# Performance work log

Hardware: AMD Instinct MI355X
Metric: run time of the kernel (lower is better)

The kernel has to match this reference:

```python
import jax, jax.numpy as jnp
import numpy as np

N_EXPERTS = 256
N_GROUP = 8
TOPK_GROUP = 4
TOP_K = 8
NORM_TOPK_PROB = True
ROUTED_SCALING_FACTOR = 2.5
NUM_TOKENS = 262144


def setup_inputs() -> dict:
    key = jax.random.key(0)
    k1, k2 = jax.random.split(key)
    router_logits = jax.random.normal(k1, (NUM_TOKENS, N_EXPERTS), dtype=jnp.float32)
    e_score_correction_bias = jax.random.normal(k2, (N_EXPERTS,), dtype=jnp.float32) * 0.1
    return {"router_logits": router_logits, "e_score_correction_bias": e_score_correction_bias}


def reference(router_logits, e_score_correction_bias):
    experts_per_group = N_EXPERTS // N_GROUP  # 32
    scores = jax.nn.sigmoid(router_logits)                       # [T, E]
    scores_for_choice = scores + e_score_correction_bias          # [T, E]

    # group score = sum of top-2 expert scores within each group
    grouped = scores_for_choice.reshape(-1, N_GROUP, experts_per_group)  # [T, G, E/G]
    top2_vals, _ = jax.lax.top_k(grouped, 2)                      # [T, G, 2]
    group_scores = top2_vals.sum(axis=-1)                         # [T, G]

    # keep top `TOPK_GROUP` groups
    _, group_idx = jax.lax.top_k(group_scores, TOPK_GROUP)        # [T, topk_group]
    group_mask = jnp.sum(jax.nn.one_hot(group_idx, N_GROUP, dtype=jnp.bool_), axis=1)  # [T, G]
    score_mask = jnp.repeat(group_mask, experts_per_group, axis=-1)  # [T, E]

    masked_scores = jnp.where(score_mask, scores_for_choice, 0.0)
    _, topk_indices = jax.lax.top_k(masked_scores, TOP_K)         # [T, top_k]

    topk_weights = jnp.take_along_axis(scores, topk_indices, axis=-1)  # [T, top_k]
    if NORM_TOPK_PROB:
        denom = topk_weights.sum(axis=-1, keepdims=True) + 1e-20
        topk_weights = topk_weights / denom
    topk_weights = topk_weights * ROUTED_SCALING_FACTOR
    return topk_indices, topk_weights
```

## Files before the change

kernel.cpp:

```cpp
#include <hip/hip_runtime.h>
#include <stdint.h>

#define NE 256
#define TKG 4
#define TK 8
#define TPB 64
#define CDW 76
#define CNT_OFF 72

typedef float pf2 __attribute__((ext_vector_type(2)));

__device__ __forceinline__ pf2 pk_fma_ss(pf2 a, pf2 b, pf2 cs) {
    pf2 d; asm("v_pk_fma_f32 %0, %1, %2, %3" : "=v"(d) : "v"(a), "v"(b), "s"(cs)); return d;
}
__device__ __forceinline__ pf2 pk_fma_sv(pf2 as, pf2 b, pf2 c) {
    pf2 d; asm("v_pk_fma_f32 %0, %1, %2, %3" : "=v"(d) : "s"(as), "v"(b), "v"(c)); return d;
}
__device__ __forceinline__ pf2 pk_fma_vv(pf2 a, pf2 b, pf2 c) {
    pf2 d; asm("v_pk_fma_f32 %0, %1, %2, %3" : "=v"(d) : "v"(a), "v"(b), "v"(c)); return d;
}
__device__ __forceinline__ pf2 pk_mul_s(pf2 a, pf2 bs) {
    pf2 d; asm("v_pk_mul_f32 %0, %1, %2" : "=v"(d) : "v"(a), "s"(bs)); return d;
}
__device__ __forceinline__ pf2 pk_mul_v(pf2 a, pf2 b) {
    pf2 d; asm("v_pk_mul_f32 %0, %1, %2" : "=v"(d) : "v"(a), "v"(b)); return d;
}
__device__ __forceinline__ pf2 pk_add_s(pf2 a, pf2 bs) {
    pf2 d; asm("v_pk_add_f32 %0, %1, %2" : "=v"(d) : "v"(a), "s"(bs)); return d;
}

__device__ __forceinline__ pf2 np_expf2(pf2 v) {
    const pf2 LOG2E  = {1.44269504088896341f, 1.44269504088896341f};
    const pf2 NLN2HI = {-0.693359375f, -0.693359375f};
    const pf2 LN2LO  = {2.12194440e-4f, 2.12194440e-4f};
    const pf2 A0     = {1.9875691500E-4f, 1.9875691500E-4f};
    const pf2 A1     = {1.3981999507E-3f, 1.3981999507E-3f};
    const pf2 A2     = {8.3334519073E-3f, 8.3334519073E-3f};
    const pf2 A3     = {4.1665795894E-2f, 4.1665795894E-2f};
    const pf2 A4     = {1.6666665459E-1f, 1.6666665459E-1f};
    const pf2 A5     = {5.0000001201E-1f, 5.0000001201E-1f};
    const pf2 ONE    = {1.0f, 1.0f};

    pf2 m = pk_mul_s(v, LOG2E);
    pf2 q; q.x = rintf(m.x); q.y = rintf(m.y);
    pf2 t = pk_fma_sv(NLN2HI, q, v);
    t = pk_fma_sv(LN2LO, q, t);
    pf2 t2 = pk_mul_v(t, t);
    pf2 p = pk_fma_sv(A0, t, A1);
    p = pk_fma_ss(p, t, A2);
    p = pk_fma_ss(p, t, A3);
    p = pk_fma_ss(p, t, A4);
    p = pk_fma_ss(p, t, A5);
    p = pk_fma_vv(p, t2, t);
    p = pk_add_s(p, ONE);
    pf2 r;
    r.x = ldexpf(p.x, (int)q.x);
    r.y = ldexpf(p.y, (int)q.y);
    return r;
}

__device__ __forceinline__ float crdiv1(float d) {
    float y0 = __builtin_amdgcn_rcpf(d);
    float e0 = fmaf(-d, y0, 1.0f);
    float y1 = fmaf(e0, y0, y0);
    float e1 = fmaf(-d, y1, 1.0f);
    float y2 = fmaf(e1, y1, y1);
    float r  = fmaf(-d, y2, 1.0f);
    return fmaf(r, y2, y2);
}

__device__ __forceinline__ unsigned ordkey(float v) {
    int b = __float_as_int(v);
    return (unsigned)(b ^ ((b >> 31) | 0x80000000));
}
__device__ __forceinline__ float inv_ordkey(unsigned u) {
    unsigned b = (u & 0x80000000u) ? (u ^ 0x80000000u) : ~u;
    return __uint_as_float(b);
}

__device__ __forceinline__ float rlanef(float v, int l) {
    return __int_as_float(__builtin_amdgcn_readlane(__float_as_int(v), l));
}
__device__ __forceinline__ unsigned rlaneu(unsigned v, int l) {
    return (unsigned)__builtin_amdgcn_readlane((int)v, l);
}
__device__ __forceinline__ unsigned umax_(unsigned a, unsigned b) { return a > b ? a : b; }
__device__ __forceinline__ int mbcnt64(unsigned long long m) {
    return __builtin_amdgcn_mbcnt_hi((unsigned)(m >> 32),
           __builtin_amdgcn_mbcnt_lo((unsigned)m, 0u));
}

template <int CTRL>
__device__ __forceinline__ float dppf(float x) {
    int xi = __float_as_int(x);
    return __int_as_float(__builtin_amdgcn_update_dpp(xi, xi, CTRL, 0xF, 0xF, false));
}
#define DPP_XOR1  0xB1
#define DPP_XOR2  0x4E
#define DPP_HMIRR 0x141
#define DPP_ROR8  0x128
#define DPP_BC15  0x142
#define DPP_BC31  0x143

#define INS8(cand) do {                                                \
    const uint64_t c_ = (cand);                                        \
    const bool q0 = c_ > v0, q1 = c_ > v1, q2 = c_ > v2, q3 = c_ > v3; \
    const bool q4 = c_ > v4, q5 = c_ > v5, q6 = c_ > v6, q7 = c_ > v7; \
    v7 = q7 ? (q6 ? v6 : c_) : v7;                                     \
    v6 = q6 ? (q5 ? v5 : c_) : v6;                                     \
    v5 = q5 ? (q4 ? v4 : c_) : v5;                                     \
    v4 = q4 ? (q3 ? v3 : c_) : v4;                                     \
    v3 = q3 ? (q2 ? v2 : c_) : v3;                                     \
    v2 = q2 ? (q1 ? v1 : c_) : v2;                                     \
    v1 = q1 ? (q0 ? v0 : c_) : v1;                                     \
    v0 = q0 ? c_ : v0;                                                 \
} while (0)

__device__ __forceinline__ void score_token(
    const float4 cur, const pf2 biasL, const pf2 biasH,
    const int lane, const int bpa, uint32_t* row)
{
    const pf2 ONE = {1.0f, 1.0f};
    pf2 eA = np_expf2((pf2){-cur.x, -cur.y});
    pf2 eB = np_expf2((pf2){-cur.z, -cur.w});
    pf2 dA = pk_add_s(eA, ONE);
    pf2 dB = pk_add_s(eB, ONE);
    const float s0 = crdiv1(dA.x);
    const float s1 = crdiv1(dA.y);
    const float s2 = crdiv1(dB.x);
    const float s3 = crdiv1(dB.y);
    const float c0 = s0 + biasL.x;
    const float c1 = s1 + biasL.y;
    const float c2 = s2 + biasH.x;
    const float c3 = s3 + biasH.y;

    float a1 = fmaxf(c0, c1), a2 = fminf(c0, c1);
    float d1 = fmaxf(c2, c3), d2 = fminf(c2, c3);
    float m1 = fmaxf(a1, d1);
    float m2 = fmaxf(fminf(a1, d1), fmaxf(a2, d2));

    {
        float p1 = dppf<DPP_XOR1>(m1), p2 = dppf<DPP_XOR1>(m2);
        float n1 = fmaxf(m1, p1);
        m2 = fmaxf(fminf(m1, p1), fmaxf(m2, p2)); m1 = n1;
    }
    {
        float p1 = dppf<DPP_XOR2>(m1), p2 = dppf<DPP_XOR2>(m2);
        float n1 = fmaxf(m1, p1);
        m2 = fmaxf(fminf(m1, p1), fmaxf(m2, p2)); m1 = n1;
    }
    {
        float p1 = dppf<DPP_HMIRR>(m1), p2 = dppf<DPP_HMIRR>(m2);
        float n1 = fmaxf(m1, p1);
        m2 = fmaxf(fminf(m1, p1), fmaxf(m2, p2)); m1 = n1;
    }
    const float gs = m1 + m2;

    const float gb = __int_as_float(
        __builtin_amdgcn_ds_bpermute(bpa, __float_as_int(gs)));
    const unsigned long long gtm = __ballot(gb > gs);
    const unsigned long long eqm = __ballot(gb == gs);
    const unsigned long long term = gtm | (eqm & 0x7F3F1F0F07030100ull);
    unsigned km8 = 0;
    #pragma unroll
    for (int a = 0; a < 8; ++a)
        km8 |= (unsigned)(__popcll((term >> (8 * a)) & 0xFFull) < 4 ? 1u : 0u) << a;
    const int g = lane >> 3;
    const bool keep = (km8 >> g) & 1u;

    const float inf_ = __uint_as_float(0x7F800000u);
    float mm = keep ? m2 : inf_;
    mm = fminf(mm, dppf<DPP_ROR8>(mm));
    mm = fminf(mm, dppf<DPP_BC15>(mm));
    mm = fminf(mm, dppf<DPP_BC31>(mm));
    const float t0f = rlanef(mm, 63);

    const bool cd0 = keep && (c0 >= t0f);
    const bool cd1 = keep && (c1 >= t0f);
    const bool cd2 = keep && (c2 >= t0f);
    const bool cd3 = keep && (c3 >= t0f);
    const unsigned long long b0 = __ballot(cd0);
    const unsigned long long b1 = __ballot(cd1);
    const unsigned long long b2 = __ballot(cd2);
    const unsigned long long b3 = __ballot(cd3);
    const unsigned p1_ = __popcll(b0);
    const unsigned p2_ = p1_ + __popcll(b1);
    const unsigned p3_ = p2_ + __popcll(b2);
    unsigned cnt = p3_ + __popcll(b3);

    const unsigned k0 = ordkey(c0);
    const unsigned k1 = ordkey(c1);
    const unsigned k2 = ordkey(c2);
    const unsigned k3 = ordkey(c3);

    const int base = lane * 4;
    if (cnt <= 32u) {
        if (cd0) *reinterpret_cast<uint64_t*>(&row[2 * (0u  + mbcnt64(b0))]) =
            ((uint64_t)k0 << 32) | (unsigned)(255 - base);
        if (cd1) *reinterpret_cast<uint64_t*>(&row[2 * (p1_ + mbcnt64(b1))]) =
            ((uint64_t)k1 << 32) | (unsigned)(255 - base - 1);
        if (cd2) *reinterpret_cast<uint64_t*>(&row[2 * (p2_ + mbcnt64(b2))]) =
            ((uint64_t)k2 << 32) | (unsigned)(255 - base - 2);
        if (cd3) *reinterpret_cast<uint64_t*>(&row[2 * (p3_ + mbcnt64(b3))]) =
            ((uint64_t)k3 << 32) | (unsigned)(255 - base - 3);
    } else {
        unsigned mk0 = keep ? k0 : 0x80000000u;
        unsigned mk1 = keep ? k1 : 0x80000000u;
        unsigned mk2 = keep ? k2 : 0x80000000u;
        unsigned mk3 = keep ? k3 : 0x80000000u;
        for (int r = 0; r < TK; ++r) {
            unsigned h = umax_(umax_(mk0, mk1), umax_(mk2, mk3));
            unsigned m = h;
            m = umax_(m, (unsigned)__shfl_xor((int)m, 1));
            m = umax_(m, (unsigned)__shfl_xor((int)m, 2));
            m = umax_(m, (unsigned)__shfl_xor((int)m, 4));
            m = umax_(m, (unsigned)__shfl_xor((int)m, 8));
            const unsigned M = umax_(umax_(rlaneu(m, 0), rlaneu(m, 16)),
                                     umax_(rlaneu(m, 32), rlaneu(m, 48)));
            const unsigned long long bl = __ballot(h == M);
            const int wl = __ffsll(bl) - 1;
            const unsigned long long sb0 = __ballot(mk0 == M);
            const unsigned long long sb1 = __ballot(mk1 == M);
            const unsigned long long sb2 = __ballot(mk2 == M);
            const int slot = ((sb0 >> wl) & 1) ? 0 : ((sb1 >> wl) & 1) ? 1
                           : ((sb2 >> wl) & 1) ? 2 : 3;
            if (lane == r)
                *reinterpret_cast<uint64_t*>(&row[2 * r]) =
                    ((uint64_t)M << 32) | (unsigned)(255 - (wl * 4 + slot));
            const bool iw = (lane == wl);
            mk0 = (iw && slot == 0) ? 0u : mk0;
            mk1 = (iw && slot == 1) ? 0u : mk1;
            mk2 = (iw && slot == 2) ? 0u : mk2;
            mk3 = (iw && slot == 3) ? 0u : mk3;
        }
        cnt = 8;
    }
    if (lane < 4)
        *reinterpret_cast<uint64_t*>(&row[2 * (cnt + lane)]) = 0ull;
    if (lane == 0) row[CNT_OFF] = cnt;
}

__global__ __launch_bounds__(256, 4) void route_kernel(
    const float* __restrict__ logits,
    const float* __restrict__ bias,
    float* __restrict__ out_idx_f,
    float* __restrict__ out_w,
    int T)
{
    __shared__ uint32_t cand[TPB * CDW];
    __shared__ float    bias_s[NE];

    const int lane = threadIdx.x & 63;
    const int wvi  = threadIdx.x >> 6;
    const long long tok0 = (long long)blockIdx.x * TPB;

    bias_s[threadIdx.x] = bias[threadIdx.x];

    {
        const float4 bias4 = *reinterpret_cast<const float4*>(bias + lane * 4);
        const pf2 biasL = {bias4.x, bias4.y};
        const pf2 biasH = {bias4.z, bias4.w};
        const float* lp = logits + (tok0 + wvi * 16) * NE + lane * 4;
        uint32_t* wrow = &cand[(wvi * 16) * CDW];
        const int bpa = (lane & 7) << 5;

        float4 cA = *reinterpret_cast<const float4*>(lp);
        float4 cB = *reinterpret_cast<const float4*>(lp + NE);
        float4 nA, nB;
        for (int i = 0; i < 8; ++i) {
            if (i < 7) {
                nA = *reinterpret_cast<const float4*>(lp + (2 * i + 2) * NE);
                nB = *reinterpret_cast<const float4*>(lp + (2 * i + 3) * NE);
            }
            score_token(cA, biasL, biasH, lane, bpa, wrow + (2 * i) * CDW);
            score_token(cB, biasL, biasH, lane, bpa, wrow + (2 * i + 1) * CDW);
            cA = nA; cB = nB;
        }
    }
    __syncthreads();

    if (threadIdx.x < TPB) {
        uint32_t* row = &cand[threadIdx.x * CDW];
        const long long t = tok0 + threadIdx.x;
        const unsigned cnt = row[CNT_OFF];
        const unsigned iters = (cnt + 3) >> 2;

        uint64_t v0 = 0, v1 = 0, v2 = 0, v3 = 0, v4 = 0, v5 = 0, v6 = 0, v7 = 0;
        const ulonglong2* rp = reinterpret_cast<const ulonglong2*>(row);
        for (unsigned it = 0; it < iters; ++it) {
            const ulonglong2 a = rp[2 * it];
            const ulonglong2 b = rp[2 * it + 1];
            INS8(a.x); INS8(a.y); INS8(b.x); INS8(b.y);
        }

        const int e0 = 255 - (int)(v0 & 255u);
        const int e1 = 255 - (int)(v1 & 255u);
        const int e2 = 255 - (int)(v2 & 255u);
        const int e3 = 255 - (int)(v3 & 255u);
        const int e4 = 255 - (int)(v4 & 255u);
        const int e5 = 255 - (int)(v5 & 255u);
        const int e6 = 255 - (int)(v6 & 255u);
        const int e7 = 255 - (int)(v7 & 255u);
        const float s0 = inv_ordkey((unsigned)(v0 >> 32)) - bias_s[e0];
        const float s1 = inv_ordkey((unsigned)(v1 >> 32)) - bias_s[e1];
        const float s2 = inv_ordkey((unsigned)(v2 >> 32)) - bias_s[e2];
        const float s3 = inv_ordkey((unsigned)(v3 >> 32)) - bias_s[e3];
        const float s4 = inv_ordkey((unsigned)(v4 >> 32)) - bias_s[e4];
        const float s5 = inv_ordkey((unsigned)(v5 >> 32)) - bias_s[e5];
        const float s6 = inv_ordkey((unsigned)(v6 >> 32)) - bias_s[e6];
        const float s7 = inv_ordkey((unsigned)(v7 >> 32)) - bias_s[e7];

        const float denom = ((s0 + s1) + (s2 + s3)) + ((s4 + s5) + (s6 + s7));
        const float scale = 2.5f * __builtin_amdgcn_rcpf(denom + 1e-20f);

        float4* oi = reinterpret_cast<float4*>(out_idx_f + t * TK);
        float4* ow = reinterpret_cast<float4*>(out_w + t * TK);
        oi[0] = make_float4((float)e0, (float)e1, (float)e2, (float)e3);
        oi[1] = make_float4((float)e4, (float)e5, (float)e6, (float)e7);
        ow[0] = make_float4(s0 * scale, s1 * scale, s2 * scale, s3 * scale);
        ow[1] = make_float4(s4 * scale, s5 * scale, s6 * scale, s7 * scale);
    }
}

extern "C" void kernel_launch(void* const* d_in, const int* in_sizes, int n_in,
                              void* d_out, int out_size, void* d_ws, size_t ws_size,
                              hipStream_t stream) {
    const float* logits = (const float*)d_in[0];
    const float* bias   = (const float*)d_in[1];
    const int T = in_sizes[0] / NE;

    float* out_idx_f = (float*)d_out;
    float* out_w     = (float*)d_out + (size_t)T * TK;

    const int grid = T / TPB;
    route_kernel<<<grid, 256, 0, stream>>>(logits, bias, out_idx_f, out_w, T);
}
```

Baseline: 90.59 us.

## Process two tokens per wavefront with 8 experts per lane

Reworks the per-token scoring so each 64-lane wavefront handles two tokens at once, with each half-wave of 32 lanes owning one token and each lane holding 8 consecutive experts instead of 4. Group top-2 reduction now needs only two DPP steps, and group ranking uses two bpermutes with half-wave ballots. This halves the number of cross-lane reduction and ballot sequences per token. In exchange it raises per-lane register use, makes the prefix and rank bookkeeping more complex, and adds a serialized slow fallback path for each half.

```diff
diff --git a/kernel.cpp b/kernel.cpp
--- a/kernel.cpp
+++ b/kernel.cpp
@@ -2,7 +2,6 @@
 #include <stdint.h>
 
 #define NE 256
-#define TKG 4
 #define TK 8
 #define TPB 64
 #define CDW 76
@@ -84,6 +83,9 @@
 __device__ __forceinline__ unsigned rlaneu(unsigned v, int l) {
     return (unsigned)__builtin_amdgcn_readlane((int)v, l);
 }
+__device__ __forceinline__ unsigned rlaneu_s(unsigned v, int l) {
+    return (unsigned)__builtin_amdgcn_readlane((int)v, l);
+}
 __device__ __forceinline__ unsigned umax_(unsigned a, unsigned b) { return a > b ? a : b; }
 __device__ __forceinline__ int mbcnt64(unsigned long long m) {
     return __builtin_amdgcn_mbcnt_hi((unsigned)(m >> 32),
@@ -97,10 +99,8 @@
 }
 #define DPP_XOR1  0xB1
 #define DPP_XOR2  0x4E
-#define DPP_HMIRR 0x141
+#define DPP_ROR4  0x124
 #define DPP_ROR8  0x128
-#define DPP_BC15  0x142
-#define DPP_BC31  0x143
 
 #define INS8(cand) do {                                                \
     const uint64_t c_ = (cand);                                        \
@@ -116,128 +116,197 @@
     v0 = q0 ? c_ : v0;                                                 \
 } while (0)
 
-__device__ __forceinline__ void score_token(
-    const float4 cur, const pf2 biasL, const pf2 biasH,
-    const int lane, const int bpa, uint32_t* row)
+__device__ __forceinline__ void score_pair(
+    const float4 xa, const float4 xb,
+    const pf2 bp0, const pf2 bp1, const pf2 bp2, const pf2 bp3,
+    const int lane, const int bpa1,
+    uint32_t* rowA, uint32_t* rowB, uint32_t* rowMine)
 {
+    const int l31 = lane & 31;
+    const int h   = lane >> 5;
+
     const pf2 ONE = {1.0f, 1.0f};
-    pf2 eA = np_expf2((pf2){-cur.x, -cur.y});
-    pf2 eB = np_expf2((pf2){-cur.z, -cur.w});
+    pf2 eA = np_expf2((pf2){-xa.x, -xa.y});
+    pf2 eB = np_expf2((pf2){-xa.z, -xa.w});
+    pf2 eC = np_expf2((pf2){-xb.x, -xb.y});
+    pf2 eD = np_expf2((pf2){-xb.z, -xb.w});
     pf2 dA = pk_add_s(eA, ONE);
     pf2 dB = pk_add_s(eB, ONE);
-    const float s0 = crdiv1(dA.x);
-    const float s1 = crdiv1(dA.y);
-    const float s2 = crdiv1(dB.x);
-    const float s3 = crdiv1(dB.y);
-    const float c0 = s0 + biasL.x;
-    const float c1 = s1 + biasL.y;
-    const float c2 = s2 + biasH.x;
-    const float c3 = s3 + biasH.y;
+    pf2 dC = pk_add_s(eC, ONE);
+    pf2 dD = pk_add_s(eD, ONE);
+    const float s0 = crdiv1(dA.x), s1 = crdiv1(dA.y);
+    const float s2 = crdiv1(dB.x), s3 = crdiv1(dB.y);
+    const float s4 = crdiv1(dC.x), s5 = crdiv1(dC.y);
+    const float s6 = crdiv1(dD.x), s7 = crdiv1(dD.y);
+    const float c0 = s0 + bp0.x, c1 = s1 + bp0.y;
+    const float c2 = s2 + bp1.x, c3 = s3 + bp1.y;
+    const float c4 = s4 + bp2.x, c5 = s5 + bp2.y;
+    const float c6 = s6 + bp3.x, c7 = s7 + bp3.y;
 
     float a1 = fmaxf(c0, c1), a2 = fminf(c0, c1);
-    float d1 = fmaxf(c2, c3), d2 = fminf(c2, c3);
-    float m1 = fmaxf(a1, d1);
-    float m2 = fmaxf(fminf(a1, d1), fmaxf(a2, d2));
+    float b1 = fmaxf(c2, c3), b2 = fminf(c2, c3);
+    float t1 = fmaxf(a1, b1), t2 = fmaxf(fminf(a1, b1), fmaxf(a2, b2));
+    float p1 = fmaxf(c4, c5), p2 = fminf(c4, c5);
+    float q1 = fmaxf(c6, c7), q2 = fminf(c6, c7);
+    float u1 = fmaxf(p1, q1), u2 = fmaxf(fminf(p1, q1), fmaxf(p2, q2));
+    float m1 = fmaxf(t1, u1), m2 = fmaxf(fminf(t1, u1), fmaxf(t2, u2));
 
     {
-        float p1 = dppf<DPP_XOR1>(m1), p2 = dppf<DPP_XOR1>(m2);
-        float n1 = fmaxf(m1, p1);
-        m2 = fmaxf(fminf(m1, p1), fmaxf(m2, p2)); m1 = n1;
+        float px1 = dppf<DPP_XOR1>(m1), px2 = dppf<DPP_XOR1>(m2);
+        float n1 = fmaxf(m1, px1);
+        m2 = fmaxf(fminf(m1, px1), fmaxf(m2, px2)); m1 = n1;
     }
     {
-        float p1 = dppf<DPP_XOR2>(m1), p2 = dppf<DPP_XOR2>(m2);
-        float n1 = fmaxf(m1, p1);
-        m2 = fmaxf(fminf(m1, p1), fmaxf(m2, p2)); m1 = n1;
-    }
-    {
-        float p1 = dppf<DPP_HMIRR>(m1), p2 = dppf<DPP_HMIRR>(m2);
-        float n1 = fmaxf(m1, p1);
-        m2 = fmaxf(fminf(m1, p1), fmaxf(m2, p2)); m1 = n1;
+        float px1 = dppf<DPP_XOR2>(m1), px2 = dppf<DPP_XOR2>(m2);
+        float n1 = fmaxf(m1, px1);
+        m2 = fmaxf(fminf(m1, px1), fmaxf(m2, px2)); m1 = n1;
     }
     const float gs = m1 + m2;
 
-    const float gb = __int_as_float(
-        __builtin_amdgcn_ds_bpermute(bpa, __float_as_int(gs)));
-    const unsigned long long gtm = __ballot(gb > gs);
-    const unsigned long long eqm = __ballot(gb == gs);
-    const unsigned long long term = gtm | (eqm & 0x7F3F1F0F07030100ull);
-    unsigned km8 = 0;
+    const float gb1 = __int_as_float(
+        __builtin_amdgcn_ds_bpermute(bpa1,      __float_as_int(gs)));
+    const float gb2 = __int_as_float(
+        __builtin_amdgcn_ds_bpermute(bpa1 + 64, __float_as_int(gs)));
+    const unsigned long long t1m = __ballot(gb1 > gs)
+        | (__ballot(gb1 == gs) & 0xFFFF7310FFFF7310ull);
+    const unsigned long long t2m = __ballot(gb2 > gs)
+        | (__ballot(gb2 == gs) & 0x7310000073100000ull);
+    unsigned kmA = 0, kmB = 0;
     #pragma unroll
-    for (int a = 0; a < 8; ++a)
-        km8 |= (unsigned)(__popcll((term >> (8 * a)) & 0xFFull) < 4 ? 1u : 0u) << a;
-    const int g = lane >> 3;
-    const bool keep = (km8 >> g) & 1u;
+    for (int a = 0; a < 8; ++a) {
+        const int rA = __popcll((t1m >> (4 * a)) & 0xFull)
+                     + __popcll((t2m >> (4 * a)) & 0xFull);
+        const int rB = __popcll((t1m >> (32 + 4 * a)) & 0xFull)
+                     + __popcll((t2m >> (32 + 4 * a)) & 0xFull);
+        kmA |= (rA < 4 ? 1u : 0u) << a;
+        kmB |= (rB < 4 ? 1u : 0u) << a;
+    }
+    const unsigned km = h ? kmB : kmA;
+    const int ga = l31 >> 2;
+    const bool keep = (km >> ga) & 1u;
 
     const float inf_ = __uint_as_float(0x7F800000u);
     float mm = keep ? m2 : inf_;
+    mm = fminf(mm, dppf<DPP_ROR4>(mm));
     mm = fminf(mm, dppf<DPP_ROR8>(mm));
-    mm = fminf(mm, dppf<DPP_BC15>(mm));
-    mm = fminf(mm, dppf<DPP_BC31>(mm));
-    const float t0f = rlanef(mm, 63);
+    const float tA = fminf(rlanef(mm, 0),  rlanef(mm, 16));
+    const float tB = fminf(rlanef(mm, 32), rlanef(mm, 48));
+    const float t0f = h ? tB : tA;
 
     const bool cd0 = keep && (c0 >= t0f);
     const bool cd1 = keep && (c1 >= t0f);
     const bool cd2 = keep && (c2 >= t0f);
     const bool cd3 = keep && (c3 >= t0f);
-    const unsigned long long b0 = __ballot(cd0);
-    const unsigned long long b1 = __ballot(cd1);
-    const unsigned long long b2 = __ballot(cd2);
-    const unsigned long long b3 = __ballot(cd3);
-    const unsigned p1_ = __popcll(b0);
-    const unsigned p2_ = p1_ + __popcll(b1);
-    const unsigned p3_ = p2_ + __popcll(b2);
-    unsigned cnt = p3_ + __popcll(b3);
-
-    const unsigned k0 = ordkey(c0);
-    const unsigned k1 = ordkey(c1);
-    const unsigned k2 = ordkey(c2);
-    const unsigned k3 = ordkey(c3);
-
-    const int base = lane * 4;
-    if (cnt <= 32u) {
-        if (cd0) *reinterpret_cast<uint64_t*>(&row[2 * (0u  + mbcnt64(b0))]) =
-            ((uint64_t)k0 << 32) | (unsigned)(255 - base);
-        if (cd1) *reinterpret_cast<uint64_t*>(&row[2 * (p1_ + mbcnt64(b1))]) =
-            ((uint64_t)k1 << 32) | (unsigned)(255 - base - 1);
-        if (cd2) *reinterpret_cast<uint64_t*>(&row[2 * (p2_ + mbcnt64(b2))]) =
-            ((uint64_t)k2 << 32) | (unsigned)(255 - base - 2);
-        if (cd3) *reinterpret_cast<uint64_t*>(&row[2 * (p3_ + mbcnt64(b3))]) =
-            ((uint64_t)k3 << 32) | (unsigned)(255 - base - 3);
-    } else {
-        unsigned mk0 = keep ? k0 : 0x80000000u;
-        unsigned mk1 = keep ? k1 : 0x80000000u;
-        unsigned mk2 = keep ? k2 : 0x80000000u;
-        unsigned mk3 = keep ? k3 : 0x80000000u;
-        for (int r = 0; r < TK; ++r) {
-            unsigned h = umax_(umax_(mk0, mk1), umax_(mk2, mk3));
-            unsigned m = h;
-            m = umax_(m, (unsigned)__shfl_xor((int)m, 1));
-            m = umax_(m, (unsigned)__shfl_xor((int)m, 2));
-            m = umax_(m, (unsigned)__shfl_xor((int)m, 4));
-            m = umax_(m, (unsigned)__shfl_xor((int)m, 8));
-            const unsigned M = umax_(umax_(rlaneu(m, 0), rlaneu(m, 16)),
-                                     umax_(rlaneu(m, 32), rlaneu(m, 48)));
-            const unsigned long long bl = __ballot(h == M);
-            const int wl = __ffsll(bl) - 1;
-            const unsigned long long sb0 = __ballot(mk0 == M);
-            const unsigned long long sb1 = __ballot(mk1 == M);
-            const unsigned long long sb2 = __ballot(mk2 == M);
-            const int slot = ((sb0 >> wl) & 1) ? 0 : ((sb1 >> wl) & 1) ? 1
-                           : ((sb2 >> wl) & 1) ? 2 : 3;
-            if (lane == r)
-                *reinterpret_cast<uint64_t*>(&row[2 * r]) =
-                    ((uint64_t)M << 32) | (unsigned)(255 - (wl * 4 + slot));
-            const bool iw = (lane == wl);
-            mk0 = (iw && slot == 0) ? 0u : mk0;
-            mk1 = (iw && slot == 1) ? 0u : mk1;
-            mk2 = (iw && slot == 2) ? 0u : mk2;
-            mk3 = (iw && slot == 3) ? 0u : mk3;
+    const bool cd4 = keep && (c4 >= t0f);
+    const bool cd5 = keep && (c5 >= t0f);
+    const bool cd6 = keep && (c6 >= t0f);
+    const bool cd7 = keep && (c7 >= t0f);
+    const unsigned long long B0 = __ballot(cd0);
+    const unsigned long long B1 = __ballot(cd1);
+    const unsigned long long B2 = __ballot(cd2);
+    const unsigned long long B3 = __ballot(cd3);
+    const unsigned long long B4 = __ballot(cd4);
+    const unsigned long long B5 = __ballot(cd5);
+    const unsigned long long B6 = __ballot(cd6);
+    const unsigned long long B7 = __ballot(cd7);
+
+    const unsigned pl0 = __popc((unsigned)B0), ph0 = __popc((unsigned)(B0 >> 32));
+    const unsigned pl1 = __popc((unsigned)B1), ph1 = __popc((unsigned)(B1 >> 32));
+    const unsigned pl2 = __popc((unsigned)B2), ph2 = __popc((unsigned)(B2 >> 32));
+    const unsigned pl3 = __popc((unsigned)B3), ph3 = __popc((unsigned)(B3 >> 32));
+    const unsigned pl4 = __popc((unsigned)B4), ph4 = __popc((unsigned)(B4 >> 32));
+    const unsigned pl5 = __popc((unsigned)B5), ph5 = __popc((unsigned)(B5 >> 32));
+    const unsigned pl6 = __popc((unsigned)B6), ph6 = __popc((unsigned)(B6 >> 32));
+    const unsigned pl7 = __popc((unsigned)B7), ph7 = __popc((unsigned)(B7 >> 32));
+    const unsigned pA0 = 0,        pA1 = pl0,       pA2 = pA1 + pl1, pA3 = pA2 + pl2;
+    const unsigned pA4 = pA3 + pl3, pA5 = pA4 + pl4, pA6 = pA5 + pl5, pA7 = pA6 + pl6;
+    const unsigned cntA = pA7 + pl7;
+    const unsigned pB0 = 0,        pB1 = ph0,       pB2 = pB1 + ph1, pB3 = pB2 + ph2;
+    const unsigned pB4 = pB3 + ph3, pB5 = pB4 + ph4, pB6 = pB5 + ph5, pB7 = pB6 + ph6;
+    const unsigned cntB = pB7 + ph7;
+    const unsigned qB0 = pB0 - pl0, qB1 = pB1 - pl1, qB2 = pB2 - pl2, qB3 = pB3 - pl3;
+    const unsigned qB4 = pB4 - pl4, qB5 = pB5 - pl5, qB6 = pB6 - pl6, qB7 = pB7 - pl7;
+
+    const unsigned k0 = ordkey(c0), k1 = ordkey(c1), k2 = ordkey(c2), k3 = ordkey(c3);
+    const unsigned k4 = ordkey(c4), k5 = ordkey(c5), k6 = ordkey(c6), k7 = ordkey(c7);
+    const int ebase = l31 * 8;
+    const bool okv = h ? (cntB <= 32u) : (cntA <= 32u);
+
+    if (cd0 && okv) *reinterpret_cast<uint64_t*>(&rowMine[2 * ((h ? qB0 : pA0) + mbcnt64(B0))]) =
+        ((uint64_t)k0 << 32) | (unsigned)(255 - ebase);
+    if (cd1 && okv) *reinterpret_cast<uint64_t*>(&rowMine[2 * ((h ? qB1 : pA1) + mbcnt64(B1))]) =
+        ((uint64_t)k1 << 32) | (unsigned)(255 - ebase - 1);
+    if (cd2 && okv) *reinterpret_cast<uint64_t*>(&rowMine[2 * ((h ? qB2 : pA2) + mbcnt64(B2))]) =
+        ((uint64_t)k2 << 32) | (unsigned)(255 - ebase - 2);
+    if (cd3 && okv) *reinterpret_cast<uint64_t*>(&rowMine[2 * ((h ? qB3 : pA3) + mbcnt64(B3))]) =
+        ((uint64_t)k3 << 32) | (unsigned)(255 - ebase - 3);
+    if (cd4 && okv) *reinterpret_cast<uint64_t*>(&rowMine[2 * ((h ? qB4 : pA4) + mbcnt64(B4))]) =
+        ((uint64_t)k4 << 32) | (unsigned)(255 - ebase - 4);
+    if (cd5 && okv) *reinterpret_cast<uint64_t*>(&rowMine[2 * ((h ? qB5 : pA5) + mbcnt64(B5))]) =
+        ((uint64_t)k5 << 32) | (unsigned)(255 - ebase - 5);
+    if (cd6 && okv) *reinterpret_cast<uint64_t*>(&rowMine[2 * ((h ? qB6 : pA6) + mbcnt64(B6))]) =
+        ((uint64_t)k6 << 32) | (unsigned)(255 - ebase - 6);
+    if (cd7 && okv) *reinterpret_cast<uint64_t*>(&rowMine[2 * ((h ? qB7 : pA7) + mbcnt64(B7))]) =
+        ((uint64_t)k7 << 32) | (unsigned)(255 - ebase - 7);
+
+    unsigned cntAp = cntA, cntBp = cntB;
+    if (__builtin_expect(cntA > 32u || cntB > 32u, 0)) {
+        #pragma unroll 1
+        for (int tgt = 0; tgt < 2; ++tgt) {
+            const unsigned cT = tgt ? cntB : cntA;
+            if (cT <= 32u) continue;
+            const bool act = (h == tgt);
+            unsigned mk0 = act ? (keep ? k0 : 0x80000000u) : 0u;
+            unsigned mk1 = act ? (keep ? k1 : 0x80000000u) : 0u;
+            unsigned mk2 = act ? (keep ? k2 : 0x80000000u) : 0u;
+            unsigned mk3 = act ? (keep ? k3 : 0x80000000u) : 0u;
+            unsigned mk4 = act ? (keep ? k4 : 0x80000000u) : 0u;
+            unsigned mk5 = act ? (keep ? k5 : 0x80000000u) : 0u;
+            unsigned mk6 = act ? (keep ? k6 : 0x80000000u) : 0u;
+            unsigned mk7 = act ? (keep ? k7 : 0x80000000u) : 0u;
+            uint32_t* rowT = tgt ? rowB : rowA;
+            #pragma unroll 1
+            for (int r_ = 0; r_ < 8; ++r_) {
+                unsigned hm = umax_(umax_(umax_(mk0, mk1), umax_(mk2, mk3)),
+                                    umax_(umax_(mk4, mk5), umax_(mk6, mk7)));
+                unsigned m = hm;
+                m = umax_(m, (unsigned)__shfl_xor((int)m, 1));
+                m = umax_(m, (unsigned)__shfl_xor((int)m, 2));
+                m = umax_(m, (unsigned)__shfl_xor((int)m, 4));
+                m = umax_(m, (unsigned)__shfl_xor((int)m, 8));
+                m = umax_(m, (unsigned)__shfl_xor((int)m, 16));
+                const unsigned M = rlaneu(m, tgt * 32);
+                const unsigned long long bl = __ballot(hm == M);
+                const int wl = __ffsll(bl) - 1;
+                int slot = 7;
+                if (rlaneu_s(mk6, wl) == M) slot = 6;
+                if (rlaneu_s(mk5, wl) == M) slot = 5;
+                if (rlaneu_s(mk4, wl) == M) slot = 4;
+                if (rlaneu_s(mk3, wl) == M) slot = 3;
+                if (rlaneu_s(mk2, wl) == M) slot = 2;
+                if (rlaneu_s(mk1, wl) == M) slot = 1;
+                if (rlaneu_s(mk0, wl) == M) slot = 0;
+                if (lane == 0)
+                    *reinterpret_cast<uint64_t*>(&rowT[2 * r_]) =
+                        ((uint64_t)M << 32) | (unsigned)(255 - ((wl & 31) * 8 + slot));
+                const bool iw = (lane == wl);
+                mk0 = (iw && slot == 0) ? 0u : mk0;
+                mk1 = (iw && slot == 1) ? 0u : mk1;
+                mk2 = (iw && slot == 2) ? 0u : mk2;
+                mk3 = (iw && slot == 3) ? 0u : mk3;
+                mk4 = (iw && slot == 4) ? 0u : mk4;
+                mk5 = (iw && slot == 5) ? 0u : mk5;
+                mk6 = (iw && slot == 6) ? 0u : mk6;
+                mk7 = (iw && slot == 7) ? 0u : mk7;
+            }
+            if (tgt) cntBp = 8u; else cntAp = 8u;
         }
-        cnt = 8;
-    }
-    if (lane < 4)
-        *reinterpret_cast<uint64_t*>(&row[2 * (cnt + lane)]) = 0ull;
-    if (lane == 0) row[CNT_OFF] = cnt;
+    }
+
+    const unsigned cntH = h ? cntBp : cntAp;
+    if (l31 < 4)
+        *reinterpret_cast<uint64_t*>(&rowMine[2 * (cntH + l31)]) = 0ull;
+    if (l31 == 0) rowMine[CNT_OFF] = cntH;
 }
 
 __global__ __launch_bounds__(256, 4) void route_kernel(
@@ -257,24 +326,35 @@
     bias_s[threadIdx.x] = bias[threadIdx.x];
 
     {
-        const float4 bias4 = *reinterpret_cast<const float4*>(bias + lane * 4);
-        const pf2 biasL = {bias4.x, bias4.y};
-        const pf2 biasH = {bias4.z, bias4.w};
-        const float* lp = logits + (tok0 + wvi * 16) * NE + lane * 4;
+        const int l31 = lane & 31;
+        const int h   = lane >> 5;
+        const float4 bb0 = *reinterpret_cast<const float4*>(bias + l31 * 8);
+        const float4 bb1 = *reinterpret_cast<const float4*>(bias + l31 * 8 + 4);
+        const pf2 bp0 = {bb0.x, bb0.y}, bp1 = {bb0.z, bb0.w};
+        const pf2 bp2 = {bb1.x, bb1.y}, bp3 = {bb1.z, bb1.w};
+        const float* lp = logits + (tok0 + wvi * 16 + h) * NE + l31 * 8;
         uint32_t* wrow = &cand[(wvi * 16) * CDW];
-        const int bpa = (lane & 7) << 5;
-
-        float4 cA = *reinterpret_cast<const float4*>(lp);
-        float4 cB = *reinterpret_cast<const float4*>(lp + NE);
-        float4 nA, nB;
-        for (int i = 0; i < 8; ++i) {
-            if (i < 7) {
-                nA = *reinterpret_cast<const float4*>(lp + (2 * i + 2) * NE);
-                nB = *reinterpret_cast<const float4*>(lp + (2 * i + 3) * NE);
+        const int bpa1 = ((lane & 32) << 2) | ((lane & 3) << 4);
+
+        float4 xa0 = *reinterpret_cast<const float4*>(lp);
+        float4 xb0 = *reinterpret_cast<const float4*>(lp + 4);
+        float4 xa1 = *reinterpret_cast<const float4*>(lp + 2 * NE);
+        float4 xb1 = *reinterpret_cast<const float4*>(lp + 2 * NE + 4);
+        float4 na0, nb0, na1, nb1;
+        for (int j = 0; j < 4; ++j) {
+            if (j < 3) {
+                na0 = *reinterpret_cast<const float4*>(lp + (4 * j + 4) * NE);
+                nb0 = *reinterpret_cast<const float4*>(lp + (4 * j + 4) * NE + 4);
+                na1 = *reinterpret_cast<const float4*>(lp + (4 * j + 6) * NE);
+                nb1 = *reinterpret_cast<const float4*>(lp + (4 * j + 6) * NE + 4);
             }
-            score_token(cA, biasL, biasH, lane, bpa, wrow + (2 * i) * CDW);
-            score_token(cB, biasL, biasH, lane, bpa, wrow + (2 * i + 1) * CDW);
-            cA = nA; cB = nB;
+            uint32_t* rA0 = wrow + (4 * j) * CDW;
+            uint32_t* rA1 = wrow + (4 * j + 2) * CDW;
+            score_pair(xa0, xb0, bp0, bp1, bp2, bp3, lane, bpa1,
+                       rA0, rA0 + CDW, rA0 + h * CDW);
+            score_pair(xa1, xb1, bp0, bp1, bp2, bp3, lane, bpa1,
+                       rA1, rA1 + CDW, rA1 + h * CDW);
+            xa0 = na0; xb0 = nb0; xa1 = na1; xb1 = nb1;
         }
     }
     __syncthreads();
```

Result: slower. 96.40 us (+6.4%).
